# Optimization experiments

Measured on AMD Instinct MI355X. Metric: run time of the kernel, lower is better.

Reference implementation:

```python
import jax, jax.numpy as jnp
import numpy as np
from jax import lax

EPS = 1e-5
DW_TH = 4.0   # threshold in cut_conv3_5_DW
PW_TH = 1e-3  # threshold in cut_conv3_5_PW


def _bn(x, gamma, beta, mean, var):
    # inference-mode batchnorm over channel dim (NCHW)
    scale = (gamma * lax.rsqrt(var + EPS))[None, :, None, None]
    shift = (beta - mean * gamma * lax.rsqrt(var + EPS))[None, :, None, None]
    return x * scale + shift


def _channel_cut(x, th):
    # faithful to max(torch.max(x[m][k]), -torch.min(x[m][k])) == max |x| per (n, c)
    max_obs = jnp.max(jnp.abs(x), axis=(2, 3), keepdims=True)  # [N, C, 1, 1]
    return jnp.where(max_obs < th, jnp.zeros_like(x), x)


def setup_inputs() -> dict:
    key = jax.random.key(0)
    ks = jax.random.split(key, 6)
    N, Cin, Cout, H, W = 32, 256, 512, 56, 56
    x = jax.random.normal(ks[0], (N, Cin, H, W), dtype=jnp.float32)
    dw_w = jax.random.normal(ks[1], (Cin, 1, 3, 3), dtype=jnp.float32) * 0.3
    dw_b = jax.random.normal(ks[2], (Cin,), dtype=jnp.float32) * 0.1
    pw_w = jax.random.normal(ks[3], (Cout, Cin), dtype=jnp.float32) * 0.05
    pw_b = jax.random.normal(ks[4], (Cout,), dtype=jnp.float32) * 0.1
    return {
        "x": x,
        "dw_w": dw_w,
        "dw_b": dw_b,
        "bn1_gamma": jnp.ones((Cin,), jnp.float32) * 2.0,
        "bn1_beta": jnp.zeros((Cin,), jnp.float32),
        "bn1_mean": jnp.zeros((Cin,), jnp.float32),
        "bn1_var": jnp.ones((Cin,), jnp.float32),
        "pw_w": pw_w,
        "pw_b": pw_b,
        "bn2_gamma": jnp.ones((Cout,), jnp.float32),
        "bn2_beta": jnp.zeros((Cout,), jnp.float32),
        "bn2_mean": jnp.zeros((Cout,), jnp.float32),
        "bn2_var": jnp.ones((Cout,), jnp.float32),
    }


def reference(x, dw_w, dw_b, bn1_gamma, bn1_beta, bn1_mean, bn1_var,
              pw_w, pw_b, bn2_gamma, bn2_beta, bn2_mean, bn2_var):
    Cin = x.shape[1]
    # depthwise 3x3 conv, padding=1 (groups == in_channels)
    y = lax.conv_general_dilated(
        x, dw_w, window_strides=(1, 1), padding=((1, 1), (1, 1)),
        dimension_numbers=("NCHW", "OIHW", "NCHW"),
        feature_group_count=Cin,
    ) + dw_b[None, :, None, None]
    y = jax.nn.relu(_bn(y, bn1_gamma, bn1_beta, bn1_mean, bn1_var))
    y = _channel_cut(y, DW_TH)
    # pointwise 1x1 conv as channel GEMM
    z = jnp.einsum("oc,nchw->nohw", pw_w, y) + pw_b[None, :, None, None]
    z = jax.nn.relu(_bn(z, bn2_gamma, bn2_beta, bn2_mean, bn2_var))
    z = _channel_cut(z, PW_TH)
    return z
```

## Files before the change

### kernel.cpp

```cpp
#include <hip/hip_runtime.h>
#include <hip/hip_bf16.h>

#define HH 56
#define WW 56
#define HW 3136
#define CIN 256
#define COUT 512
#define NBATCH 32
#define EPS 1e-5f
#define DW_TH 4.0f
#define PW_TH 1e-3f

#define CG 32
#define CPITCH 508

typedef __attribute__((ext_vector_type(8))) short s16x8;
typedef __attribute__((ext_vector_type(4))) float f32x4;
typedef unsigned int u32;
typedef unsigned short u16;

__device__ __forceinline__ void async_copy16(void* lds, const void* g) {
    __builtin_amdgcn_global_load_lds((const __attribute__((address_space(1))) unsigned int*)g,
                                     (__attribute__((address_space(3))) unsigned int*)lds,
                                     16, 0, 0);
}

__device__ __forceinline__ u16 bf16_bits(float f) {
    __hip_bfloat16 h = __float2bfloat16(f);
    union { __hip_bfloat16 h; u16 u; } cv; cv.h = h; return cv.u;
}

__global__ __launch_bounds__(256) void prep_kernel(
    const float* __restrict__ pww, const float* __restrict__ pwb,
    const float* __restrict__ g2, const float* __restrict__ b2,
    const float* __restrict__ m2, const float* __restrict__ v2,
    u16* __restrict__ wb, float2* __restrict__ scsh,
    u32* __restrict__ omax, u32* __restrict__ dwmax)
{
    const int gid = blockIdx.x * 256 + threadIdx.x;
    const int base = gid * 8;
    const float4 a = *(const float4*)(pww + base);
    const float4 b = *(const float4*)(pww + base + 4);
    union { u16 u[8]; s16x8 v; } pk;
    pk.u[0] = bf16_bits(a.x); pk.u[1] = bf16_bits(a.y);
    pk.u[2] = bf16_bits(a.z); pk.u[3] = bf16_bits(a.w);
    pk.u[4] = bf16_bits(b.x); pk.u[5] = bf16_bits(b.y);
    pk.u[6] = bf16_bits(b.z); pk.u[7] = bf16_bits(b.w);
    *(s16x8*)(wb + base) = pk.v;
    omax[gid] = 0u;
    if (gid < NBATCH * CIN) dwmax[gid] = 0u;
    if (gid < COUT) {
        const float sc = g2[gid] * rsqrtf(v2[gid] + EPS);
        const float sh = fmaf(-m2[gid], sc, b2[gid]) + pwb[gid] * sc;
        scsh[gid] = make_float2(sc, sh);
    }
}

__global__ __launch_bounds__(256) void dw_kernel(
    const float* __restrict__ x, const float* __restrict__ dww, const float* __restrict__ dwb,
    const float* __restrict__ g1, const float* __restrict__ b1,
    const float* __restrict__ m1, const float* __restrict__ v1,
    u16* __restrict__ y, u32* __restrict__ dwmax)
{
    __shared__ float xs[CG * CPITCH];

    const int bid = blockIdx.x;
    const int cg = bid & 7;
    const int hs = (bid >> 3) & 7;
    const int n  = bid >> 6;
    const int t  = threadIdx.x;

    const int g0     = hs * 7 - 1;
    const int gstart = (g0 < 0) ? 0 : g0;
    const int gend   = (hs * 7 + 7 > 55) ? 55 : hs * 7 + 7;
    const int nrows  = gend - gstart + 1;
    const int dst0   = gstart - g0;
    const int cnt4   = nrows * 14;

    if (hs == 0) {
        for (int i = t; i < CG * 14; i += 256) {
            const int c = i / 14, j = i - c * 14;
            *(float4*)&xs[c * CPITCH + j * 4] = make_float4(0.f, 0.f, 0.f, 0.f);
        }
    } else if (hs == 7) {
        for (int i = t; i < CG * 14; i += 256) {
            const int c = i / 14, j = i - c * 14;
            *(float4*)&xs[c * CPITCH + 8 * 56 + j * 4] = make_float4(0.f, 0.f, 0.f, 0.f);
        }
    }

    {
        const float* gbase = x + (size_t)(n * CIN + cg * CG) * HW + gstart * 56;
        const int half = t >> 7;
        const int i4 = t & 127;
        for (int cc = 0; cc < 16; ++cc) {
            const int c = cc * 2 + half;
            if (i4 < cnt4) {
                const float4 v = *(const float4*)(gbase + (size_t)c * HW + i4 * 4);
                *(float4*)&xs[c * CPITCH + dst0 * 56 + i4 * 4] = v;
            }
        }
    }
    __syncthreads();

    const int r = t >> 5;
    const int c = t & 31;
    float vmax = 0.f;
    if (r < 7) {
        const int ch = cg * CG + c;
        const float* wp = dww + ch * 9;
        const float w00 = wp[0], w01 = wp[1], w02 = wp[2];
        const float w10 = wp[3], w11 = wp[4], w12 = wp[5];
        const float w20 = wp[6], w21 = wp[7], w22 = wp[8];
        const float sc = g1[ch] * rsqrtf(v1[ch] + EPS);
        const float sh = fmaf(-m1[ch], sc, b1[ch]) + dwb[ch] * sc;

        const float* rm = &xs[c * CPITCH + r * 56];
        const float* r0 = rm + 56;
        const float* rp = rm + 112;
        const int grow = hs * 7 + r;
        u16* yo = y + (size_t)(n * HW + grow * WW) * CIN + ch;

        float4 cm = *(const float4*)rm;
        float4 c0 = *(const float4*)r0;
        float4 cp = *(const float4*)rp;
        float lm = 0.f, l0 = 0.f, lp = 0.f;

        for (int chk = 0; chk < 14; ++chk) {
            float4 nm, n0, np;
            if (chk < 13) {
                nm = *(const float4*)(rm + 4 * chk + 4);
                n0 = *(const float4*)(r0 + 4 * chk + 4);
                np = *(const float4*)(rp + 4 * chk + 4);
            } else {
                nm = n0 = np = make_float4(0.f, 0.f, 0.f, 0.f);
            }
            float s0 = w00*lm   + w01*cm.x + w02*cm.y
                     + w10*l0   + w11*c0.x + w12*c0.y
                     + w20*lp   + w21*cp.x + w22*cp.y;
            float s1 = w00*cm.x + w01*cm.y + w02*cm.z
                     + w10*c0.x + w11*c0.y + w12*c0.z
                     + w20*cp.x + w21*cp.y + w22*cp.z;
            float s2 = w00*cm.y + w01*cm.z + w02*cm.w
                     + w10*c0.y + w11*c0.z + w12*c0.w
                     + w20*cp.y + w21*cp.z + w22*cp.w;
            float s3 = w00*cm.z + w01*cm.w + w02*nm.x
                     + w10*c0.z + w11*c0.w + w12*n0.x
                     + w20*cp.z + w21*cp.w + w22*np.x;
            const float v0 = fmaxf(fmaf(s0, sc, sh), 0.f);
            const float v1s = fmaxf(fmaf(s1, sc, sh), 0.f);
            const float v2s = fmaxf(fmaf(s2, sc, sh), 0.f);
            const float v3 = fmaxf(fmaf(s3, sc, sh), 0.f);
            vmax = fmaxf(fmaxf(vmax, fmaxf(v0, v1s)), fmaxf(v2s, v3));
            yo[(4 * chk + 0) * CIN] = bf16_bits(v0);
            yo[(4 * chk + 1) * CIN] = bf16_bits(v1s);
            yo[(4 * chk + 2) * CIN] = bf16_bits(v2s);
            yo[(4 * chk + 3) * CIN] = bf16_bits(v3);
            lm = cm.w; l0 = c0.w; lp = cp.w;
            cm = nm; c0 = n0; cp = np;
        }
    }
    vmax = fmaxf(vmax, __shfl_xor(vmax, 32));
    if ((t & 32) == 0)
        atomicMax(&dwmax[n * CIN + cg * CG + c], __float_as_uint(vmax));
}

__global__ __launch_bounds__(256, 2) void pw_kernel(
    const u16* __restrict__ y, const u16* __restrict__ wb,
    const float2* __restrict__ scsh, const u32* __restrict__ dwmax,
    float* __restrict__ out, u32* __restrict__ omax)
{
    __shared__ __align__(16) u16 Wt[2][256 * 32];
    __shared__ __align__(16) u16 Yt[2][112 * 32];
    __shared__ __align__(16) u16 msk[CIN];

    const int bid = blockIdx.x;
    const int g   = (bid & 7) * 224 + (bid >> 3);
    const int ot  = g & 1;
    const int r2  = g >> 1;
    const int hwt = r2 % 28;
    const int n   = r2 / 28;

    const int t = threadIdx.x;
    const int w = t >> 6;
    const int l = t & 63;
    const int lo = l & 15, hi = l >> 4;

    const int o_blk  = ot * 256;
    const int hw_blk = n * HW + hwt * 112;

    const u16* wg = wb + (size_t)(o_blk + w * 64 + (l >> 2)) * CIN + (l & 3) * 8;
    const u16* yg = y  + (size_t)(hw_blk + (l >> 2)) * CIN + (l & 3) * 8;

    msk[t] = (__uint_as_float(dwmax[n * CIN + t]) >= DW_TH) ? (u16)0xFFFFu : (u16)0u;

    f32x4 acc[4][7];
#pragma unroll
    for (int s = 0; s < 4; ++s)
#pragma unroll
        for (int j = 0; j < 7; ++j) acc[s][j] = (f32x4){0.f, 0.f, 0.f, 0.f};

    {
        char* WtB = (char*)&Wt[0][0];
        char* YtB = (char*)&Yt[0][0];
#pragma unroll
        for (int i = 0; i < 4; ++i)
            async_copy16(WtB + (w * 64 + i * 16) * 64 + l * 16, wg + (size_t)(i * 16) * CIN);
        const int j0 = 2 * w;
        async_copy16(YtB + (j0 * 16) * 64 + l * 16, yg + (size_t)(j0 * 16) * CIN);
        if (j0 + 1 < 7)
            async_copy16(YtB + ((j0 + 1) * 16) * 64 + l * 16, yg + (size_t)((j0 + 1) * 16) * CIN);
    }
    __syncthreads();

#pragma unroll 2
    for (int tk = 0; tk < 8; ++tk) {
        const int cur = tk & 1;
        if (tk < 7) {
            const int k1 = (tk + 1) * 32;
            char* WtB = (char*)&Wt[cur ^ 1][0];
            char* YtB = (char*)&Yt[cur ^ 1][0];
#pragma unroll
            for (int i = 0; i < 4; ++i)
                async_copy16(WtB + (w * 64 + i * 16) * 64 + l * 16, wg + k1 + (size_t)(i * 16) * CIN);
            const int j0 = 2 * w;
            async_copy16(YtB + (j0 * 16) * 64 + l * 16, yg + k1 + (size_t)(j0 * 16) * CIN);
            if (j0 + 1 < 7)
                async_copy16(YtB + ((j0 + 1) * 16) * 64 + l * 16, yg + k1 + (size_t)((j0 + 1) * 16) * CIN);
        }
        const char* WtB = (const char*)&Wt[cur][0];
        const char* YtB = (const char*)&Yt[cur][0];
        const s16x8 m8 = *(const s16x8*)((const char*)msk + tk * 64 + hi * 16);

        s16x8 af[4], bf[7];
#pragma unroll
        for (int s = 0; s < 4; ++s) {
            af[s] = *(const s16x8*)(WtB + (w * 64 + s * 16 + lo) * 64 + hi * 16);
            af[s] = af[s] & m8;
        }
#pragma unroll
        for (int j = 0; j < 7; ++j)
            bf[j] = *(const s16x8*)(YtB + (j * 16 + lo) * 64 + hi * 16);
#pragma unroll
        for (int s = 0; s < 4; ++s)
#pragma unroll
            for (int j = 0; j < 7; ++j)
                acc[s][j] = __builtin_amdgcn_mfma_f32_16x16x32_bf16(af[s], bf[j], acc[s][j], 0, 0, 0);
        __syncthreads();
    }

#pragma unroll
    for (int s = 0; s < 4; ++s) {
#pragma unroll
        for (int r = 0; r < 4; ++r) {
            const int o = o_blk + w * 64 + s * 16 + hi * 4 + r;
            const float2 ss = scsh[o];
            float m = 0.f;
            float* op = out + (size_t)(n * COUT + o) * HW + hwt * 112 + lo;
#pragma unroll
            for (int j = 0; j < 7; ++j) {
                const float v = fmaxf(fmaf(acc[s][j][r], ss.x, ss.y), 0.f);
                op[j * 16] = v;
                m = fmaxf(m, v);
            }
            m = fmaxf(m, __shfl_xor(m, 1));
            m = fmaxf(m, __shfl_xor(m, 2));
            m = fmaxf(m, __shfl_xor(m, 4));
            m = fmaxf(m, __shfl_xor(m, 8));
            if (lo == 0) atomicMax(&omax[n * COUT + o], __float_as_uint(m));
        }
    }
}

__global__ __launch_bounds__(256) void pwcut_kernel(const u32* __restrict__ omax, float* __restrict__ out)
{
    const int b = blockIdx.x;
    if (__uint_as_float(omax[b]) >= PW_TH) return;
    float* p = out + (size_t)b * HW;
    for (int i = threadIdx.x; i < HW; i += 256) p[i] = 0.0f;
}

extern "C" void kernel_launch(void* const* d_in, const int* in_sizes, int n_in,
                              void* d_out, int out_size, void* d_ws, size_t ws_size,
                              hipStream_t stream) {
    const float* x   = (const float*)d_in[0];
    const float* dww = (const float*)d_in[1];
    const float* dwb = (const float*)d_in[2];
    const float* g1  = (const float*)d_in[3];
    const float* b1  = (const float*)d_in[4];
    const float* m1  = (const float*)d_in[5];
    const float* v1  = (const float*)d_in[6];
    const float* pww = (const float*)d_in[7];
    const float* pwb = (const float*)d_in[8];
    const float* g2  = (const float*)d_in[9];
    const float* b2  = (const float*)d_in[10];
    const float* m2  = (const float*)d_in[11];
    const float* v2  = (const float*)d_in[12];
    float* out = (float*)d_out;

    u32*    omax  = (u32*)d_ws;
    u32*    dwmax = (u32*)((char*)d_ws + (64 << 10));
    float2* scsh  = (float2*)((char*)d_ws + (96 << 10));
    u16*    wbf   = (u16*)((char*)d_ws + (128 << 10));
    u16*    y     = (u16*)((char*)d_ws + (1 << 20));

    prep_kernel<<<64, 256, 0, stream>>>(pww, pwb, g2, b2, m2, v2, wbf, scsh, omax, dwmax);
    dw_kernel<<<NBATCH * 8 * 8, 256, 0, stream>>>(x, dww, dwb, g1, b1, m1, v1, y, dwmax);
    pw_kernel<<<1792, 256, 0, stream>>>(y, wbf, scsh, dwmax, out, omax);
    pwcut_kernel<<<NBATCH * COUT, 256, 0, stream>>>(omax, out);
}
```

Before: 373.7 us.

## Fuse prep into depthwise kernel, triple-buffer GEMM, replace atomics with partial maxima

```diff
diff --git a/kernel.cpp b/kernel.cpp
--- a/kernel.cpp
+++ b/kernel.cpp
@@ -1,8 +1,6 @@
 #include <hip/hip_runtime.h>
 #include <hip/hip_bf16.h>
 
-#define HH 56
-#define WW 56
 #define HW 3136
 #define CIN 256
 #define COUT 512
@@ -11,8 +9,7 @@
 #define DW_TH 4.0f
 #define PW_TH 1e-3f
 
-#define CG 32
-#define CPITCH 508
+#define DPITCH 564
 
 typedef __attribute__((ext_vector_type(8))) short s16x8;
 typedef __attribute__((ext_vector_type(4))) float f32x4;
@@ -30,75 +27,74 @@
     union { __hip_bfloat16 h; u16 u; } cv; cv.h = h; return cv.u;
 }
 
-__global__ __launch_bounds__(256) void prep_kernel(
-    const float* __restrict__ pww, const float* __restrict__ pwb,
-    const float* __restrict__ g2, const float* __restrict__ b2,
-    const float* __restrict__ m2, const float* __restrict__ v2,
-    u16* __restrict__ wb, float2* __restrict__ scsh,
-    u32* __restrict__ omax, u32* __restrict__ dwmax)
-{
-    const int gid = blockIdx.x * 256 + threadIdx.x;
-    const int base = gid * 8;
-    const float4 a = *(const float4*)(pww + base);
-    const float4 b = *(const float4*)(pww + base + 4);
-    union { u16 u[8]; s16x8 v; } pk;
-    pk.u[0] = bf16_bits(a.x); pk.u[1] = bf16_bits(a.y);
-    pk.u[2] = bf16_bits(a.z); pk.u[3] = bf16_bits(a.w);
-    pk.u[4] = bf16_bits(b.x); pk.u[5] = bf16_bits(b.y);
-    pk.u[6] = bf16_bits(b.z); pk.u[7] = bf16_bits(b.w);
-    *(s16x8*)(wb + base) = pk.v;
-    omax[gid] = 0u;
-    if (gid < NBATCH * CIN) dwmax[gid] = 0u;
-    if (gid < COUT) {
-        const float sc = g2[gid] * rsqrtf(v2[gid] + EPS);
-        const float sh = fmaf(-m2[gid], sc, b2[gid]) + pwb[gid] * sc;
-        scsh[gid] = make_float2(sc, sh);
-    }
-}
-
 __global__ __launch_bounds__(256) void dw_kernel(
     const float* __restrict__ x, const float* __restrict__ dww, const float* __restrict__ dwb,
     const float* __restrict__ g1, const float* __restrict__ b1,
     const float* __restrict__ m1, const float* __restrict__ v1,
-    u16* __restrict__ y, u32* __restrict__ dwmax)
+    const float* __restrict__ pww, const float* __restrict__ pwb,
+    const float* __restrict__ g2, const float* __restrict__ b2,
+    const float* __restrict__ m2, const float* __restrict__ v2,
+    u16* __restrict__ y, float* __restrict__ dwmaxp,
+    u16* __restrict__ wb, float2* __restrict__ scsh)
 {
-    __shared__ float xs[CG * CPITCH];
-
     const int bid = blockIdx.x;
-    const int cg = bid & 7;
-    const int hs = (bid >> 3) & 7;
-    const int n  = bid >> 6;
-    const int t  = threadIdx.x;
-
-    const int g0     = hs * 7 - 1;
+    const int t = threadIdx.x;
+
+    if (bid >= 1792) {
+        const int gid = (bid - 1792) * 256 + t;
+        const int base = gid * 8;
+        const float4 a = *(const float4*)(pww + base);
+        const float4 b = *(const float4*)(pww + base + 4);
+        union { u16 u[8]; s16x8 v; } pk;
+        pk.u[0] = bf16_bits(a.x); pk.u[1] = bf16_bits(a.y);
+        pk.u[2] = bf16_bits(a.z); pk.u[3] = bf16_bits(a.w);
+        pk.u[4] = bf16_bits(b.x); pk.u[5] = bf16_bits(b.y);
+        pk.u[6] = bf16_bits(b.z); pk.u[7] = bf16_bits(b.w);
+        *(s16x8*)(wb + base) = pk.v;
+        if (gid < COUT) {
+            const float sc = g2[gid] * rsqrtf(v2[gid] + EPS);
+            const float sh = fmaf(-m2[gid], sc, b2[gid]) + pwb[gid] * sc;
+            scsh[gid] = make_float2(sc, sh);
+        }
+        return;
+    }
+
+    __shared__ float xs[32 * DPITCH];
+    __shared__ float sm[256];
+
+    const int n   = bid / 56;
+    const int rem = bid % 56;
+    const int hs  = rem >> 3;
+    const int cg  = rem & 7;
+
+    const int g0     = hs * 8 - 1;
     const int gstart = (g0 < 0) ? 0 : g0;
-    const int gend   = (hs * 7 + 7 > 55) ? 55 : hs * 7 + 7;
-    const int nrows  = gend - gstart + 1;
-    const int dst0   = gstart - g0;
+    const int nrows  = (hs == 0 || hs == 6) ? 9 : 10;
+    const int dst0   = (hs == 0) ? 1 : 0;
     const int cnt4   = nrows * 14;
 
     if (hs == 0) {
-        for (int i = t; i < CG * 14; i += 256) {
+        for (int i = t; i < 32 * 14; i += 256) {
             const int c = i / 14, j = i - c * 14;
-            *(float4*)&xs[c * CPITCH + j * 4] = make_float4(0.f, 0.f, 0.f, 0.f);
-        }
-    } else if (hs == 7) {
-        for (int i = t; i < CG * 14; i += 256) {
+            *(float4*)&xs[c * DPITCH + j * 4] = make_float4(0.f, 0.f, 0.f, 0.f);
+        }
+    } else if (hs == 6) {
+        for (int i = t; i < 32 * 14; i += 256) {
             const int c = i / 14, j = i - c * 14;
-            *(float4*)&xs[c * CPITCH + 8 * 56 + j * 4] = make_float4(0.f, 0.f, 0.f, 0.f);
+            *(float4*)&xs[c * DPITCH + 9 * 56 + j * 4] = make_float4(0.f, 0.f, 0.f, 0.f);
         }
     }
 
     {
-        const float* gbase = x + (size_t)(n * CIN + cg * CG) * HW + gstart * 56;
-        const int half = t >> 7;
-        const int i4 = t & 127;
-        for (int cc = 0; cc < 16; ++cc) {
-            const int c = cc * 2 + half;
-            if (i4 < cnt4) {
-                const float4 v = *(const float4*)(gbase + (size_t)c * HW + i4 * 4);
-                *(float4*)&xs[c * CPITCH + dst0 * 56 + i4 * 4] = v;
-            }
+        const float* gbase = x + (size_t)(n * CIN + cg * 32) * HW + gstart * 56;
+        const int w = t >> 6, lane = t & 63;
+        for (int i = 0; i < 24; ++i) {
+            const int j = w + 4 * i;
+            const int c = j / 3, s = j - c * 3;
+            const int i4 = s * 64 + lane;
+            if (i4 < cnt4)
+                async_copy16(&xs[c * DPITCH + dst0 * 56 + i4 * 4],
+                             gbase + (size_t)c * HW + i4 * 4);
         }
     }
     __syncthreads();
@@ -106,8 +102,8 @@
     const int r = t >> 5;
     const int c = t & 31;
     float vmax = 0.f;
-    if (r < 7) {
-        const int ch = cg * CG + c;
+    {
+        const int ch = cg * 32 + c;
         const float* wp = dww + ch * 9;
         const float w00 = wp[0], w01 = wp[1], w02 = wp[2];
         const float w10 = wp[3], w11 = wp[4], w12 = wp[5];
@@ -115,11 +111,11 @@
         const float sc = g1[ch] * rsqrtf(v1[ch] + EPS);
         const float sh = fmaf(-m1[ch], sc, b1[ch]) + dwb[ch] * sc;
 
-        const float* rm = &xs[c * CPITCH + r * 56];
+        const float* rm = &xs[c * DPITCH + r * 56];
         const float* r0 = rm + 56;
         const float* rp = rm + 112;
-        const int grow = hs * 7 + r;
-        u16* yo = y + (size_t)(n * HW + grow * WW) * CIN + ch;
+        const int grow = hs * 8 + r;
+        u16* yo = y + (size_t)(n * HW + grow * 56) * CIN + ch;
 
         float4 cm = *(const float4*)rm;
         float4 c0 = *(const float4*)r0;
@@ -147,10 +143,10 @@
             float s3 = w00*cm.z + w01*cm.w + w02*nm.x
                      + w10*c0.z + w11*c0.w + w12*n0.x
                      + w20*cp.z + w21*cp.w + w22*np.x;
-            const float v0 = fmaxf(fmaf(s0, sc, sh), 0.f);
+            const float v0  = fmaxf(fmaf(s0, sc, sh), 0.f);
             const float v1s = fmaxf(fmaf(s1, sc, sh), 0.f);
             const float v2s = fmaxf(fmaf(s2, sc, sh), 0.f);
-            const float v3 = fmaxf(fmaf(s3, sc, sh), 0.f);
+            const float v3  = fmaxf(fmaf(s3, sc, sh), 0.f);
             vmax = fmaxf(fmaxf(vmax, fmaxf(v0, v1s)), fmaxf(v2s, v3));
             yo[(4 * chk + 0) * CIN] = bf16_bits(v0);
             yo[(4 * chk + 1) * CIN] = bf16_bits(v1s);
@@ -160,18 +156,24 @@
             cm = nm; c0 = n0; cp = np;
         }
     }
-    vmax = fmaxf(vmax, __shfl_xor(vmax, 32));
-    if ((t & 32) == 0)
-        atomicMax(&dwmax[n * CIN + cg * CG + c], __float_as_uint(vmax));
+
+    sm[t] = vmax;
+    __syncthreads();
+    if (t < 32) {
+        float m = sm[t];
+#pragma unroll
+        for (int k = 1; k < 8; ++k) m = fmaxf(m, sm[t + 32 * k]);
+        dwmaxp[(n * 7 + hs) * 256 + cg * 32 + t] = m;
+    }
 }
 
 __global__ __launch_bounds__(256, 2) void pw_kernel(
     const u16* __restrict__ y, const u16* __restrict__ wb,
-    const float2* __restrict__ scsh, const u32* __restrict__ dwmax,
-    float* __restrict__ out, u32* __restrict__ omax)
+    const float2* __restrict__ scsh, const float* __restrict__ dwmaxp,
+    float* __restrict__ out, float* __restrict__ omaxp)
 {
-    __shared__ __align__(16) u16 Wt[2][256 * 32];
-    __shared__ __align__(16) u16 Yt[2][112 * 32];
+    __shared__ __align__(16) u16 Wt[3][256 * 32];
+    __shared__ __align__(16) u16 Yt[3][128 * 32];
     __shared__ __align__(16) u16 msk[CIN];
 
     const int bid = blockIdx.x;
@@ -192,7 +194,13 @@
     const u16* wg = wb + (size_t)(o_blk + w * 64 + (l >> 2)) * CIN + (l & 3) * 8;
     const u16* yg = y  + (size_t)(hw_blk + (l >> 2)) * CIN + (l & 3) * 8;
 
-    msk[t] = (__uint_as_float(dwmax[n * CIN + t]) >= DW_TH) ? (u16)0xFFFFu : (u16)0u;
+    {
+        float mm = dwmaxp[n * 7 * 256 + t];
+#pragma unroll
+        for (int s2 = 1; s2 < 7; ++s2) mm = fmaxf(mm, dwmaxp[(n * 7 + s2) * 256 + t]);
+        msk[t] = (mm >= DW_TH) ? (u16)0xFFFFu : (u16)0u;
+    }
+    __syncthreads();
 
     f32x4 acc[4][7];
 #pragma unroll
@@ -200,39 +208,39 @@
 #pragma unroll
         for (int j = 0; j < 7; ++j) acc[s][j] = (f32x4){0.f, 0.f, 0.f, 0.f};
 
-    {
-        char* WtB = (char*)&Wt[0][0];
-        char* YtB = (char*)&Yt[0][0];
-#pragma unroll
-        for (int i = 0; i < 4; ++i)
-            async_copy16(WtB + (w * 64 + i * 16) * 64 + l * 16, wg + (size_t)(i * 16) * CIN);
-        const int j0 = 2 * w;
-        async_copy16(YtB + (j0 * 16) * 64 + l * 16, yg + (size_t)(j0 * 16) * CIN);
-        if (j0 + 1 < 7)
-            async_copy16(YtB + ((j0 + 1) * 16) * 64 + l * 16, yg + (size_t)((j0 + 1) * 16) * CIN);
-    }
-    __syncthreads();
-
-#pragma unroll 2
+#define STAGE(buf, k0) do {                                                            \
+        char* WtB_ = (char*)&Wt[buf][0];                                               \
+        char* YtB_ = (char*)&Yt[buf][0];                                               \
+        _Pragma("unroll")                                                              \
+        for (int i_ = 0; i_ < 4; ++i_)                                                 \
+            async_copy16(WtB_ + (w * 64 + i_ * 16) * 64 + l * 16,                      \
+                         wg + (k0) + (size_t)(i_ * 16) * CIN);                         \
+        const int j0_ = 2 * w;                                                         \
+        async_copy16(YtB_ + (j0_ * 16) * 64 + l * 16,                                  \
+                     yg + (k0) + (size_t)(j0_ * 16) * CIN);                            \
+        const int j1_ = j0_ + 1, sj_ = (j1_ == 7) ? 6 : j1_;                           \
+        async_copy16(YtB_ + (j1_ * 16) * 64 + l * 16,                                  \
+                     yg + (k0) + (size_t)(sj_ * 16) * CIN);                            \
+    } while (0)
+
+    STAGE(0, 0);
+    asm volatile("" ::: "memory");
+    STAGE(1, 32);
+
+#pragma unroll
     for (int tk = 0; tk < 8; ++tk) {
-        const int cur = tk & 1;
-        if (tk < 7) {
-            const int k1 = (tk + 1) * 32;
-            char* WtB = (char*)&Wt[cur ^ 1][0];
-            char* YtB = (char*)&Yt[cur ^ 1][0];
-#pragma unroll
-            for (int i = 0; i < 4; ++i)
-                async_copy16(WtB + (w * 64 + i * 16) * 64 + l * 16, wg + k1 + (size_t)(i * 16) * CIN);
-            const int j0 = 2 * w;
-            async_copy16(YtB + (j0 * 16) * 64 + l * 16, yg + k1 + (size_t)(j0 * 16) * CIN);
-            if (j0 + 1 < 7)
-                async_copy16(YtB + ((j0 + 1) * 16) * 64 + l * 16, yg + k1 + (size_t)((j0 + 1) * 16) * CIN);
-        }
+        const int cur = tk % 3;
+        if (tk < 7) asm volatile("s_waitcnt vmcnt(6)" ::: "memory");
+        else        asm volatile("s_waitcnt vmcnt(0)" ::: "memory");
+        __builtin_amdgcn_s_barrier();
+        __builtin_amdgcn_sched_barrier(0);
+        if (tk < 6) { STAGE((tk + 2) % 3, (tk + 2) * 32); }
+
         const char* WtB = (const char*)&Wt[cur][0];
         const char* YtB = (const char*)&Yt[cur][0];
         const s16x8 m8 = *(const s16x8*)((const char*)msk + tk * 64 + hi * 16);
 
-        s16x8 af[4], bf[7];
+        s16x8 af[4], bf7[7];
 #pragma unroll
         for (int s = 0; s < 4; ++s) {
             af[s] = *(const s16x8*)(WtB + (w * 64 + s * 16 + lo) * 64 + hi * 16);
@@ -240,14 +248,17 @@
         }
 #pragma unroll
         for (int j = 0; j < 7; ++j)
-            bf[j] = *(const s16x8*)(YtB + (j * 16 + lo) * 64 + hi * 16);
+            bf7[j] = *(const s16x8*)(YtB + (j * 16 + lo) * 64 + hi * 16);
+
+        __builtin_amdgcn_s_setprio(1);
 #pragma unroll
         for (int s = 0; s < 4; ++s)
 #pragma unroll
             for (int j = 0; j < 7; ++j)
-                acc[s][j] = __builtin_amdgcn_mfma_f32_16x16x32_bf16(af[s], bf[j], acc[s][j], 0, 0, 0);
-        __syncthreads();
-    }
+                acc[s][j] = __builtin_amdgcn_mfma_f32_16x16x32_bf16(af[s], bf7[j], acc[s][j], 0, 0, 0);
+        __builtin_amdgcn_s_setprio(0);
+    }
+#undef STAGE
 
 #pragma unroll
     for (int s = 0; s < 4; ++s) {
@@ -267,17 +278,22 @@
             m = fmaxf(m, __shfl_xor(m, 2));
             m = fmaxf(m, __shfl_xor(m, 4));
             m = fmaxf(m, __shfl_xor(m, 8));
-            if (lo == 0) atomicMax(&omax[n * COUT + o], __float_as_uint(m));
-        }
-    }
-}
-
-__global__ __launch_bounds__(256) void pwcut_kernel(const u32* __restrict__ omax, float* __restrict__ out)
+            if (lo == 0) omaxp[(size_t)(n * COUT + o) * 28 + hwt] = m;
+        }
+    }
+}
+
+__global__ __launch_bounds__(64) void pwcut_kernel(const float* __restrict__ omaxp, float* __restrict__ out)
 {
     const int b = blockIdx.x;
-    if (__uint_as_float(omax[b]) >= PW_TH) return;
-    float* p = out + (size_t)b * HW;
-    for (int i = threadIdx.x; i < HW; i += 256) p[i] = 0.0f;
+    const int t = threadIdx.x;
+    float m = (t < 28) ? omaxp[(size_t)b * 28 + t] : 0.f;
+#pragma unroll
+    for (int d = 1; d < 64; d <<= 1) m = fmaxf(m, __shfl_xor(m, d));
+    if (m >= PW_TH) return;
+    float4* p = (float4*)(out + (size_t)b * HW);
+    const float4 z = make_float4(0.f, 0.f, 0.f, 0.f);
+    for (int i = t; i < HW / 4; i += 64) p[i] = z;
 }
 
 extern "C" void kernel_launch(void* const* d_in, const int* in_sizes, int n_in,
@@ -298,14 +314,15 @@
     const float* v2  = (const float*)d_in[12];
     float* out = (float*)d_out;
 
-    u32*    omax  = (u32*)d_ws;
-    u32*    dwmax = (u32*)((char*)d_ws + (64 << 10));
-    float2* scsh  = (float2*)((char*)d_ws + (96 << 10));
-    u16*    wbf   = (u16*)((char*)d_ws + (128 << 10));
-    u16*    y     = (u16*)((char*)d_ws + (1 << 20));
-
-    prep_kernel<<<64, 256, 0, stream>>>(pww, pwb, g2, b2, m2, v2, wbf, scsh, omax, dwmax);
-    dw_kernel<<<NBATCH * 8 * 8, 256, 0, stream>>>(x, dww, dwb, g1, b1, m1, v1, y, dwmax);
-    pw_kernel<<<1792, 256, 0, stream>>>(y, wbf, scsh, dwmax, out, omax);
-    pwcut_kernel<<<NBATCH * COUT, 256, 0, stream>>>(omax, out);
-}
+    float*  omaxp  = (float*)d_ws;
+    float*  dwmaxp = (float*)((char*)d_ws + (2 << 20));
+    float2* scsh   = (float2*)((char*)d_ws + (3 << 20));
+    u16*    wbf    = (u16*)((char*)d_ws + (4 << 20));
+    u16*    yv     = (u16*)((char*)d_ws + (8 << 20));
+
+    dw_kernel<<<1792 + 64, 256, 0, stream>>>(x, dww, dwb, g1, b1, m1, v1,
+                                             pww, pwb, g2, b2, m2, v2,
+                                             yv, dwmaxp, wbf, scsh);
+    pw_kernel<<<1792, 256, 0, stream>>>(yv, wbf, scsh, dwmaxp, out, omaxp);
+    pwcut_kernel<<<NBATCH * COUT, 64, 0, stream>>>(omaxp, out);
+}
```

After: 368.8 us. No clear change (-1.3%).
